# Kernel tuning notes

Hardware: AMD Instinct MI355X
Metric: run time of the kernel (lower is better)

Reference implementation:

```python
import jax, jax.numpy as jnp
import numpy as np
import math

L = 6      # num transformer layers
D = 128    # hidden_dim
H = 8      # heads
C = D // H # per-head dim (concat -> H*C == hidden_dim so residual add works)
F = 9      # node_features
OUT = 3    # output_dim
B, S, NN = 2, 128, 64
N = B * S * NN
E = 262144


def setup_inputs() -> dict:
    key = jax.random.key(0)
    ks = jax.random.split(key, 16)
    sc = 0.02
    g = lambda k, shp: jax.random.normal(k, shp, jnp.float32) * sc

    x = jax.random.normal(ks[0], (N, F), jnp.float32)
    edge_index = jax.random.randint(ks[1], (2, E), 0, N, dtype=jnp.int32)

    # sinusoidal positional encoding buffer [S, D]
    pos = np.arange(S, dtype=np.float32)[:, None]
    div = np.exp(np.arange(0, D, 2, dtype=np.float32) * (-math.log(10000.0) / D))
    pe = np.zeros((S, D), np.float32)
    pe[:, 0::2] = np.sin(pos * div)
    pe[:, 1::2] = np.cos(pos * div)

    return dict(
        x=x, edge_index=edge_index, pe=jnp.asarray(pe),
        Win=g(ks[2], (F, D)), bin_=jnp.zeros((D,), jnp.float32),
        Wq=g(ks[3], (L, D, D)), bq=jnp.zeros((L, D), jnp.float32),
        Wk=g(ks[4], (L, D, D)), bk=jnp.zeros((L, D), jnp.float32),
        Wv=g(ks[5], (L, D, D)), bv=jnp.zeros((L, D), jnp.float32),
        Ws=g(ks[6], (L, D, D)), bs=jnp.zeros((L, D), jnp.float32),
        Wb=g(ks[7], (L, 3 * D, 1)), bb=jnp.zeros((L, 1), jnp.float32),
        ln_g=jnp.ones((L, D), jnp.float32), ln_b=jnp.zeros((L, D), jnp.float32),
        Wo1=g(ks[8], (D, D // 2)), bo1=jnp.zeros((D // 2,), jnp.float32),
        Wo2=g(ks[9], (D // 2, OUT)), bo2=jnp.zeros((OUT,), jnp.float32),
        batch_size=B, seq_len=S, num_nodes=NN,
    )


def _layer_norm(x, g, b, eps=1e-5):
    mu = x.mean(-1, keepdims=True)
    var = ((x - mu) ** 2).mean(-1, keepdims=True)
    return (x - mu) / jnp.sqrt(var + eps) * g + b


def _transformer_conv(h, src, dst, Wq, bq, Wk, bk, Wv, bv, Ws, bs, Wb, bb):
    # PyG TransformerConv (beta=True, concat): edge gather -> per-head dot scores
    # -> scatter-softmax over incoming edges per dst node -> scatter-add aggregate.
    n = h.shape[0]
    q = (h @ Wq + bq).reshape(n, H, C)
    k = (h @ Wk + bk).reshape(n, H, C)
    v = (h @ Wv + bv).reshape(n, H, C)
    scores = jnp.einsum('ehc,ehc->eh', q[dst], k[src]) / math.sqrt(C)  # [E,H]
    m = jax.ops.segment_max(scores, dst, num_segments=n)               # [N,H]
    ex = jnp.exp(scores - jax.lax.stop_gradient(m)[dst])
    denom = jax.ops.segment_sum(ex, dst, num_segments=n)
    alpha = ex / (denom[dst] + 1e-16)                                  # [E,H]
    msg = (v[src] * alpha[:, :, None]).reshape(-1, H * C)              # [E,D]
    agg = jax.ops.segment_sum(msg, dst, num_segments=n)                # [N,D]
    xr = h @ Ws + bs                                                   # skip branch
    beta = jax.nn.sigmoid(jnp.concatenate([agg, xr, agg - xr], -1) @ Wb + bb)
    return beta * xr + (1.0 - beta) * agg


def reference(x, edge_index, pe, Win, bin_, Wq, bq, Wk, bk, Wv, bv, Ws, bs,
              Wb, bb, ln_g, ln_b, Wo1, bo1, Wo2, bo2,
              batch_size, seq_len, num_nodes):
    src, dst = edge_index[0], edge_index[1]
    d = Win.shape[1]
    h = x @ Win + bin_
    # add temporal positional encoding per timestep
    h = (h.reshape(batch_size, seq_len, num_nodes, d)
         + pe[:seq_len][None, :, None, :]).reshape(-1, d)
    for i in range(Wq.shape[0]):
        hn = _transformer_conv(h, src, dst, Wq[i], bq[i], Wk[i], bk[i],
                               Wv[i], bv[i], Ws[i], bs[i], Wb[i], bb[i])
        h = _layer_norm(h + hn, ln_g[i], ln_b[i])
    return jax.nn.relu(h @ Wo1 + bo1) @ Wo2 + bo2
```

## Files before the change

### kernel.cpp

```cpp
#include <hip/hip_runtime.h>

#define NNODES 16384
#define EDGES  262144
#define DH     128
#define NH     8
#define CH     16
#define NL     6
#define SEQ    128
#define NNPG   64

typedef short bf16x8 __attribute__((ext_vector_type(8)));
typedef float f32x4 __attribute__((ext_vector_type(4)));
typedef float f32x2 __attribute__((ext_vector_type(2)));

static __device__ __forceinline__ unsigned short f2bf(float f) {
  unsigned u = __float_as_uint(f);
  u += 0x7FFFu + ((u >> 16) & 1u);
  return (unsigned short)(u >> 16);
}
static __device__ __forceinline__ float bfl(unsigned u) { return __uint_as_float(u << 16); }
static __device__ __forceinline__ float bfh(unsigned u) { return __uint_as_float(u & 0xffff0000u); }
static __device__ __forceinline__ f32x2 mk2(float x, float y) { f32x2 t; t[0] = x; t[1] = y; return t; }

__global__ __launch_bounds__(128) void k_input(const float* __restrict__ x,
    const float* __restrict__ Win, const float* __restrict__ bin,
    const float* __restrict__ pe, float* __restrict__ h,
    unsigned short* __restrict__ hb) {
  const int n = blockIdx.x, d = threadIdx.x;
  __shared__ float xs[9];
  if (d < 9) xs[d] = x[n * 9 + d];
  __syncthreads();
  float acc = bin[d];
#pragma unroll
  for (int f = 0; f < 9; ++f) acc = fmaf(xs[f], Win[f * DH + d], acc);
  const float val = acc + pe[((n / NNPG) % SEQ) * DH + d];
  h[n * DH + d] = val;
  hb[n * DH + d] = f2bf(val);
}

__global__ __launch_bounds__(256) void k_count(const int* __restrict__ ei,
                                               int* __restrict__ cnt) {
  const int e = blockIdx.x * 256 + threadIdx.x;
  atomicAdd(&cnt[ei[EDGES + e]], 1);
}

__global__ __launch_bounds__(1024) void k_scan(int* __restrict__ cnt,
                                               int* __restrict__ row_start) {
  __shared__ int part[1024];
  const int t = threadIdx.x;
  int loc[16];
  int s = 0;
  const int base = t * 16;
#pragma unroll
  for (int i = 0; i < 16; ++i) { loc[i] = cnt[base + i]; s += loc[i]; }
  part[t] = s;
  __syncthreads();
  for (int off = 1; off < 1024; off <<= 1) {
    int add = (t >= off) ? part[t - off] : 0;
    __syncthreads();
    part[t] += add;
    __syncthreads();
  }
  int run = (t == 0) ? 0 : part[t - 1];
#pragma unroll
  for (int i = 0; i < 16; ++i) {
    row_start[base + i] = run;
    run += loc[i];
    cnt[base + i] = 0;
  }
  if (t == 0) row_start[NNODES] = EDGES;
}

__global__ __launch_bounds__(256) void k_fill(const int* __restrict__ ei,
    const int* __restrict__ row_start, int* __restrict__ cursor,
    int* __restrict__ csr_src) {
  const int e = blockIdx.x * 256 + threadIdx.x;
  const int d = ei[EDGES + e];
  csr_src[row_start[d] + atomicAdd(&cursor[d], 1)] = ei[e];
}

__global__ __launch_bounds__(64) void k_wconv(const float* __restrict__ Wq,
    const float* __restrict__ Wk, const float* __restrict__ Wv,
    const float* __restrict__ Ws, unsigned short* __restrict__ Wf) {
  const int bid = blockIdx.x;
  const int layer = bid >> 7, rem = bid & 127;
  const int mat = rem >> 5, tile = rem & 31;
  const int nt = tile >> 2, kt = tile & 3;
  const int lane = threadIdx.x;
  const float* W = ((mat == 0) ? Wq : (mat == 1) ? Wk : (mat == 2) ? Wv : Ws)
                   + layer * DH * DH;
  const int n = nt * 16 + (lane & 15);
  const int k0 = kt * 32 + (lane >> 4) * 8;
  unsigned pk[4];
#pragma unroll
  for (int jj = 0; jj < 4; ++jj) {
    const unsigned lo = f2bf(W[(k0 + 2 * jj) * DH + n]);
    const unsigned hi = f2bf(W[(k0 + 2 * jj + 1) * DH + n]);
    pk[jj] = lo | (hi << 16);
  }
  uint4 o = {pk[0], pk[1], pk[2], pk[3]};
  *(uint4*)&Wf[(((layer * 4 + mat) * 32 + tile) * 64 + lane) * 8] = o;
}

__global__ __launch_bounds__(256) void k_gemm(const unsigned short* __restrict__ hb,
    const unsigned short* __restrict__ Wf,
    const float* __restrict__ bq, const float* __restrict__ bk,
    const float* __restrict__ bv, const float* __restrict__ bs,
    unsigned short* __restrict__ qb, unsigned char* __restrict__ kv8,
    float* __restrict__ xr) {
  const int mt = blockIdx.x;
  const int wv = threadIdx.x >> 6, lane = threadIdx.x & 63;
  const int g = blockIdx.y * 4 + wv;
  const int mat = g >> 1, nbase = (g & 1) * 64;
  const unsigned short* Wm = Wf + mat * 16384;
  const float* bias = (mat == 0) ? bq : (mat == 1) ? bk : (mat == 2) ? bv : bs;
  const int m0 = lane & 15, quad = lane >> 4;
  const int nt0 = (g & 1) * 4;

  const f32x4 z = {0.f, 0.f, 0.f, 0.f};
  f32x4 acc[2][4] = {{z, z, z, z}, {z, z, z, z}};
#pragma unroll
  for (int kt = 0; kt < 4; ++kt) {
    const bf16x8 a0 = *(const bf16x8*)&hb[(mt * 32 + m0) * DH + kt * 32 + quad * 8];
    const bf16x8 a1 = *(const bf16x8*)&hb[(mt * 32 + 16 + m0) * DH + kt * 32 + quad * 8];
#pragma unroll
    for (int j = 0; j < 4; ++j) {
      const bf16x8 b = *(const bf16x8*)&Wm[(((nt0 + j) * 4 + kt) * 64 + lane) * 8];
      acc[0][j] = __builtin_amdgcn_mfma_f32_16x16x32_bf16(a0, b, acc[0][j], 0, 0, 0);
      acc[1][j] = __builtin_amdgcn_mfma_f32_16x16x32_bf16(a1, b, acc[1][j], 0, 0, 0);
    }
  }
  const int kvoff = (mat == 1) ? 0 : 128;
#pragma unroll
  for (int half = 0; half < 2; ++half) {
#pragma unroll
    for (int j = 0; j < 4; ++j) {
      const int col = nbase + j * 16 + m0;
      const float bvv = bias[col];
#pragma unroll
      for (int r = 0; r < 4; ++r) {
        const float val = acc[half][j][r] + bvv;
        const int row = mt * 32 + half * 16 + quad * 4 + r;
        if (mat == 0) {
          qb[row * DH + col] = f2bf(val);
        } else if (mat == 3) {
          xr[row * DH + col] = val;
        } else {
          const float nbv = __shfl_xor(val, 1);
          if ((lane & 1) == 0) {
            const int pk = __builtin_amdgcn_cvt_pk_fp8_f32(val, nbv, 0, false);
            *(unsigned short*)&kv8[row * 256 + kvoff + col] = (unsigned short)pk;
          }
        }
      }
    }
  }
}

__device__ __forceinline__ void load16bf2(const unsigned short* __restrict__ p, f32x2* r) {
  const uint4 a = *(const uint4*)p;
  const uint4 b = *(const uint4*)(p + 8);
  r[0] = mk2(bfl(a.x), bfh(a.x)); r[1] = mk2(bfl(a.y), bfh(a.y));
  r[2] = mk2(bfl(a.z), bfh(a.z)); r[3] = mk2(bfl(a.w), bfh(a.w));
  r[4] = mk2(bfl(b.x), bfh(b.x)); r[5] = mk2(bfl(b.y), bfh(b.y));
  r[6] = mk2(bfl(b.z), bfh(b.z)); r[7] = mk2(bfl(b.w), bfh(b.w));
}

__device__ __forceinline__ void decode8x2(const uint4 u, f32x2* r) {
  r[0] = __builtin_amdgcn_cvt_pk_f32_fp8(u.x, false);
  r[1] = __builtin_amdgcn_cvt_pk_f32_fp8(u.x, true);
  r[2] = __builtin_amdgcn_cvt_pk_f32_fp8(u.y, false);
  r[3] = __builtin_amdgcn_cvt_pk_f32_fp8(u.y, true);
  r[4] = __builtin_amdgcn_cvt_pk_f32_fp8(u.z, false);
  r[5] = __builtin_amdgcn_cvt_pk_f32_fp8(u.z, true);
  r[6] = __builtin_amdgcn_cvt_pk_f32_fp8(u.w, false);
  r[7] = __builtin_amdgcn_cvt_pk_f32_fp8(u.w, true);
}

__device__ __forceinline__ void edge_acc2(const uint4 ku, const uint4 vu, bool valid,
    const f32x2* __restrict__ q2, f32x2* __restrict__ a2, float& denom) {
  f32x2 kr[8];
  decode8x2(ku, kr);
  f32x2 d2 = mk2(0.f, 0.f);
#pragma unroll
  for (int c = 0; c < 8; ++c) d2 = d2 + q2[c] * kr[c];
  const float dot = d2[0] + d2[1];
  const float ex = valid ? __expf(dot * 0.25f) : 0.f;
  denom += ex;
  f32x2 vr[8];
  decode8x2(vu, vr);
  const f32x2 e2 = mk2(ex, ex);
#pragma unroll
  for (int c = 0; c < 8; ++c) a2[c] = a2[c] + e2 * vr[c];
}

__global__ __launch_bounds__(256, 4) void k_attn_epi(const unsigned short* __restrict__ qb,
    const unsigned char* __restrict__ kv8,
    const int* __restrict__ row_start, const int* __restrict__ csr_src,
    float* __restrict__ h, unsigned short* __restrict__ hb,
    const float* __restrict__ xr,
    const float* __restrict__ Wb, const float* __restrict__ bb,
    const float* __restrict__ ln_g, const float* __restrict__ ln_b) {
  const int wv = threadIdx.x >> 6, lane = threadIdx.x & 63;
  const int n = blockIdx.x * 4 + wv;
  const int es = lane >> 3, hd = lane & 7;
  const int beg = row_start[n], end = row_start[n + 1];
  const int deg = end - beg;
  const int ntb = (deg >= 32) ? 4 : ((deg + 7) >> 3);
  const int j0 = beg + es;
  int idx[4];
#pragma unroll
  for (int t = 0; t < 4; ++t) {
    idx[t] = -1;
    if (t < ntb) {
      const int jt = j0 + 8 * t;
      if (jt < end) idx[t] = csr_src[jt];
    }
  }
  f32x2 q2[8];
  load16bf2(&qb[n * DH + hd * CH], q2);
  uint4 kf[4], vf[4];
#pragma unroll
  for (int t = 0; t < 4; ++t) {
    if (t < ntb) {
      const int s = (idx[t] >= 0) ? idx[t] : 0;
      const unsigned char* base = &kv8[s * 256 + hd * CH];
      kf[t] = *(const uint4*)base;
      vf[t] = *(const uint4*)(base + 128);
    }
  }
  f32x2 a2[8];
#pragma unroll
  for (int c = 0; c < 8; ++c) a2[c] = mk2(0.f, 0.f);
  float denom = 0.f;
#pragma unroll
  for (int t = 0; t < 4; ++t) {
    if (t < ntb) edge_acc2(kf[t], vf[t], idx[t] >= 0, q2, a2, denom);
  }
  for (int j = j0 + 32; j < end; j += 8) {
    const int s = csr_src[j];
    const unsigned char* base = &kv8[s * 256 + hd * CH];
    const uint4 ku = *(const uint4*)base;
    const uint4 vu = *(const uint4*)(base + 128);
    edge_acc2(ku, vu, true, q2, a2, denom);
  }
#pragma unroll
  for (int off = 8; off <= 32; off <<= 1) {
    denom += __shfl_xor(denom, off);
#pragma unroll
    for (int c = 0; c < 8; ++c) {
      const f32x2 t = mk2(__shfl_xor(a2[c][0], off), __shfl_xor(a2[c][1], off));
      a2[c] = a2[c] + t;
    }
  }
  const float inv = 1.f / (denom + 1e-16f);
  float o0 = 0.f, o1 = 0.f;
#pragma unroll
  for (int c = 0; c < 8; ++c) {
    if (es == c) { o0 = a2[c][0]; o1 = a2[c][1]; }
  }
  const int d0 = hd * CH + es * 2;
  const float ax = o0 * inv, ay = o1 * inv;
  const float2 r = *(const float2*)&xr[n * DH + d0];
  const float2 w0 = *(const float2*)&Wb[d0];
  const float2 w1 = *(const float2*)&Wb[DH + d0];
  const float2 w2 = *(const float2*)&Wb[2 * DH + d0];
  float p = ax * w0.x + ay * w0.y + r.x * w1.x + r.y * w1.y
          + (ax - r.x) * w2.x + (ay - r.y) * w2.y;
#pragma unroll
  for (int off = 1; off <= 32; off <<= 1) p += __shfl_xor(p, off);
  const float beta = 1.f / (1.f + __expf(-(p + bb[0])));
  const float2 hv = *(const float2*)&h[n * DH + d0];
  const float t0 = hv.x + beta * r.x + (1.f - beta) * ax;
  const float t1 = hv.y + beta * r.y + (1.f - beta) * ay;
  float sum = t0 + t1, sq = t0 * t0 + t1 * t1;
#pragma unroll
  for (int off = 1; off <= 32; off <<= 1) {
    sum += __shfl_xor(sum, off);
    sq  += __shfl_xor(sq, off);
  }
  const float mu = sum * (1.f / DH);
  const float rinv = rsqrtf(sq * (1.f / DH) - mu * mu + 1e-5f);
  const float2 g = *(const float2*)&ln_g[d0];
  const float2 b = *(const float2*)&ln_b[d0];
  float2 o = {(t0 - mu) * rinv * g.x + b.x, (t1 - mu) * rinv * g.y + b.y};
  *(float2*)&h[n * DH + d0] = o;
  const unsigned lo = f2bf(o.x), hi = f2bf(o.y);
  *(unsigned*)&hb[n * DH + d0] = lo | (hi << 16);
}

__global__ __launch_bounds__(256) void k_final(const float* __restrict__ h,
    const float* __restrict__ Wo1, const float* __restrict__ bo1,
    const float* __restrict__ Wo2, const float* __restrict__ bo2,
    float* __restrict__ out) {
  __shared__ float hs[4][DH];
  const int lane = threadIdx.x & 63, wid = threadIdx.x >> 6;
  const int n = blockIdx.x * 4 + wid;
  const float2 hv = *(const float2*)&h[n * DH + lane * 2];
  hs[wid][lane * 2] = hv.x;
  hs[wid][lane * 2 + 1] = hv.y;
  __syncthreads();
  float m = bo1[lane];
#pragma unroll 16
  for (int d = 0; d < DH; ++d) m = fmaf(hs[wid][d], Wo1[d * 64 + lane], m);
  m = fmaxf(m, 0.f);
  float o0 = m * Wo2[lane * 3 + 0];
  float o1 = m * Wo2[lane * 3 + 1];
  float o2 = m * Wo2[lane * 3 + 2];
#pragma unroll
  for (int off = 32; off; off >>= 1) {
    o0 += __shfl_xor(o0, off);
    o1 += __shfl_xor(o1, off);
    o2 += __shfl_xor(o2, off);
  }
  if (lane == 0) {
    out[n * 3 + 0] = o0 + bo2[0];
    out[n * 3 + 1] = o1 + bo2[1];
    out[n * 3 + 2] = o2 + bo2[2];
  }
}

extern "C" void kernel_launch(void* const* d_in, const int* in_sizes, int n_in,
                              void* d_out, int out_size, void* d_ws, size_t ws_size,
                              hipStream_t stream) {
  const float* x   = (const float*)d_in[0];
  const int*   ei  = (const int*)d_in[1];
  const float* pe  = (const float*)d_in[2];
  const float* Win = (const float*)d_in[3];
  const float* bin = (const float*)d_in[4];
  const float* Wq  = (const float*)d_in[5];
  const float* bq  = (const float*)d_in[6];
  const float* Wk  = (const float*)d_in[7];
  const float* bk  = (const float*)d_in[8];
  const float* Wv  = (const float*)d_in[9];
  const float* bv  = (const float*)d_in[10];
  const float* Wsk = (const float*)d_in[11];
  const float* bs  = (const float*)d_in[12];
  const float* Wb  = (const float*)d_in[13];
  const float* bb  = (const float*)d_in[14];
  const float* lng = (const float*)d_in[15];
  const float* lnb = (const float*)d_in[16];
  const float* Wo1 = (const float*)d_in[17];
  const float* bo1 = (const float*)d_in[18];
  const float* Wo2 = (const float*)d_in[19];
  const float* bo2 = (const float*)d_in[20];

  const size_t NU = (size_t)NNODES * DH;
  char* base = (char*)d_ws;
  float* h   = (float*)base;                  base += NU * 4;
  float* xr  = (float*)base;                  base += NU * 4;
  unsigned short* hb = (unsigned short*)base; base += NU * 2;
  unsigned short* qb = (unsigned short*)base; base += NU * 2;
  unsigned char* kv8 = (unsigned char*)base;  base += NU * 2;
  unsigned short* Wf = (unsigned short*)base; base += (size_t)NL * 4 * 16384 * 2;
  int* row_start = (int*)base;                base += (NNODES + 1) * 4;
  int* cnt       = (int*)base;                base += NNODES * 4;
  int* csr_src   = (int*)base;

  (void)hipMemsetAsync(cnt, 0, NNODES * sizeof(int), stream);
  k_count<<<EDGES / 256, 256, 0, stream>>>(ei, cnt);
  k_scan<<<1, 1024, 0, stream>>>(cnt, row_start);
  k_fill<<<EDGES / 256, 256, 0, stream>>>(ei, row_start, cnt, csr_src);
  k_wconv<<<NL * 128, 64, 0, stream>>>(Wq, Wk, Wv, Wsk, Wf);
  k_input<<<NNODES, 128, 0, stream>>>(x, Win, bin, pe, h, hb);
  for (int l = 0; l < NL; ++l) {
    k_gemm<<<dim3(NNODES / 32, 2), 256, 0, stream>>>(
        hb, Wf + (size_t)l * 4 * 16384,
        bq + l * DH, bk + l * DH, bv + l * DH, bs + l * DH, qb, kv8, xr);
    k_attn_epi<<<NNODES / 4, 256, 0, stream>>>(qb, kv8, row_start, csr_src,
                                               h, hb, xr, Wb + l * 3 * DH, bb + l,
                                               lng + l * DH, lnb + l * DH);
  }
  k_final<<<NNODES / 4, 256, 0, stream>>>(h, Wo1, bo1, Wo2, bo2, (float*)d_out);
}
```

Baseline: 379.5 us.

## Interleave K/V per head, pad first-32 CSR neighbors, warp-shuffle scan and reduce-scatter

Replaces the shared-memory Hillis-Steele scan with a warp-shuffle scan plus per-wave sums. It adds a padded per-node table of the first 32 neighbor indices, so each attention lane fetches its four indices with one int4 load. It also interleaves the fp8 K and V per head so both sit in the same 32-byte chunk, and swaps the butterfly all-reduce of the 16 accumulator values for a halving reduce-scatter that moves fewer shuffles. The cost is an extra memset and padded index buffer, plus a nondeterministic slot order within the padded table.

Result: no change. 376.4 us (-0.8%).

```diff
diff --git a/kernel.cpp b/kernel.cpp
--- a/kernel.cpp
+++ b/kernel.cpp
@@ -46,22 +46,29 @@
 
 __global__ __launch_bounds__(1024) void k_scan(int* __restrict__ cnt,
                                                int* __restrict__ row_start) {
-  __shared__ int part[1024];
+  __shared__ int wsum[16];
   const int t = threadIdx.x;
+  const int lane = t & 63, wid = t >> 6;
   int loc[16];
   int s = 0;
   const int base = t * 16;
 #pragma unroll
   for (int i = 0; i < 16; ++i) { loc[i] = cnt[base + i]; s += loc[i]; }
-  part[t] = s;
+  int sc = s;
+#pragma unroll
+  for (int off = 1; off <= 32; off <<= 1) {
+    const int v = __shfl_up(sc, off);
+    if (lane >= off) sc += v;
+  }
+  if (lane == 63) wsum[wid] = sc;
   __syncthreads();
-  for (int off = 1; off < 1024; off <<= 1) {
-    int add = (t >= off) ? part[t - off] : 0;
-    __syncthreads();
-    part[t] += add;
-    __syncthreads();
-  }
-  int run = (t == 0) ? 0 : part[t - 1];
+  int wbase = 0;
+#pragma unroll
+  for (int w = 0; w < 16; ++w) {
+    const int v = wsum[w];
+    if (w < wid) wbase += v;
+  }
+  int run = wbase + sc - s;
 #pragma unroll
   for (int i = 0; i < 16; ++i) {
     row_start[base + i] = run;
@@ -73,10 +80,13 @@
 
 __global__ __launch_bounds__(256) void k_fill(const int* __restrict__ ei,
     const int* __restrict__ row_start, int* __restrict__ cursor,
-    int* __restrict__ csr_src) {
+    int* __restrict__ csr_src, int* __restrict__ csr_pad) {
   const int e = blockIdx.x * 256 + threadIdx.x;
   const int d = ei[EDGES + e];
-  csr_src[row_start[d] + atomicAdd(&cursor[d], 1)] = ei[e];
+  const int s = ei[e];
+  const int slot = atomicAdd(&cursor[d], 1);
+  csr_src[row_start[d] + slot] = s;
+  if (slot < 32) csr_pad[d * 32 + (slot & 7) * 4 + (slot >> 3)] = s;
 }
 
 __global__ __launch_bounds__(64) void k_wconv(const float* __restrict__ Wq,
@@ -130,7 +140,7 @@
       acc[1][j] = __builtin_amdgcn_mfma_f32_16x16x32_bf16(a1, b, acc[1][j], 0, 0, 0);
     }
   }
-  const int kvoff = (mat == 1) ? 0 : 128;
+  const int kvoff = (mat == 1) ? 0 : 16;
 #pragma unroll
   for (int half = 0; half < 2; ++half) {
 #pragma unroll
@@ -149,7 +159,9 @@
           const float nbv = __shfl_xor(val, 1);
           if ((lane & 1) == 0) {
             const int pk = __builtin_amdgcn_cvt_pk_fp8_f32(val, nbv, 0, false);
-            *(unsigned short*)&kv8[row * 256 + kvoff + col] = (unsigned short)pk;
+            const int head = col >> 4, dim = col & 15;
+            *(unsigned short*)&kv8[row * 256 + head * 32 + kvoff + dim] =
+                (unsigned short)pk;
           }
         }
       }
@@ -197,6 +209,7 @@
 __global__ __launch_bounds__(256, 4) void k_attn_epi(const unsigned short* __restrict__ qb,
     const unsigned char* __restrict__ kv8,
     const int* __restrict__ row_start, const int* __restrict__ csr_src,
+    const int* __restrict__ csr_pad,
     float* __restrict__ h, unsigned short* __restrict__ hb,
     const float* __restrict__ xr,
     const float* __restrict__ Wb, const float* __restrict__ bb,
@@ -204,19 +217,11 @@
   const int wv = threadIdx.x >> 6, lane = threadIdx.x & 63;
   const int n = blockIdx.x * 4 + wv;
   const int es = lane >> 3, hd = lane & 7;
+  const int4 iv = *(const int4*)&csr_pad[n * 32 + es * 4];
   const int beg = row_start[n], end = row_start[n + 1];
   const int deg = end - beg;
   const int ntb = (deg >= 32) ? 4 : ((deg + 7) >> 3);
-  const int j0 = beg + es;
-  int idx[4];
-#pragma unroll
-  for (int t = 0; t < 4; ++t) {
-    idx[t] = -1;
-    if (t < ntb) {
-      const int jt = j0 + 8 * t;
-      if (jt < end) idx[t] = csr_src[jt];
-    }
-  }
+  int idx[4] = {iv.x, iv.y, iv.z, iv.w};
   f32x2 q2[8];
   load16bf2(&qb[n * DH + hd * CH], q2);
   uint4 kf[4], vf[4];
@@ -224,9 +229,9 @@
   for (int t = 0; t < 4; ++t) {
     if (t < ntb) {
       const int s = (idx[t] >= 0) ? idx[t] : 0;
-      const unsigned char* base = &kv8[s * 256 + hd * CH];
+      const unsigned char* base = &kv8[s * 256 + hd * 32];
       kf[t] = *(const uint4*)base;
-      vf[t] = *(const uint4*)(base + 128);
+      vf[t] = *(const uint4*)(base + 16);
     }
   }
   f32x2 a2[8];
@@ -237,28 +242,42 @@
   for (int t = 0; t < 4; ++t) {
     if (t < ntb) edge_acc2(kf[t], vf[t], idx[t] >= 0, q2, a2, denom);
   }
-  for (int j = j0 + 32; j < end; j += 8) {
+  for (int j = beg + es + 32; j < end; j += 8) {
     const int s = csr_src[j];
-    const unsigned char* base = &kv8[s * 256 + hd * CH];
+    const unsigned char* base = &kv8[s * 256 + hd * 32];
     const uint4 ku = *(const uint4*)base;
-    const uint4 vu = *(const uint4*)(base + 128);
+    const uint4 vu = *(const uint4*)(base + 16);
     edge_acc2(ku, vu, true, q2, a2, denom);
   }
 #pragma unroll
-  for (int off = 8; off <= 32; off <<= 1) {
-    denom += __shfl_xor(denom, off);
-#pragma unroll
-    for (int c = 0; c < 8; ++c) {
-      const f32x2 t = mk2(__shfl_xor(a2[c][0], off), __shfl_xor(a2[c][1], off));
-      a2[c] = a2[c] + t;
-    }
-  }
+  for (int off = 8; off <= 32; off <<= 1) denom += __shfl_xor(denom, off);
+  const bool hi32 = (lane & 32) != 0;
+  f32x2 r4[4];
+#pragma unroll
+  for (int c = 0; c < 4; ++c) {
+    const f32x2 keep = hi32 ? a2[c + 4] : a2[c];
+    const f32x2 send = hi32 ? a2[c] : a2[c + 4];
+    const f32x2 rec = mk2(__shfl_xor(send[0], 32), __shfl_xor(send[1], 32));
+    r4[c] = keep + rec;
+  }
+  const bool hi16 = (lane & 16) != 0;
+  f32x2 r2[2];
+#pragma unroll
+  for (int c = 0; c < 2; ++c) {
+    const f32x2 keep = hi16 ? r4[c + 2] : r4[c];
+    const f32x2 send = hi16 ? r4[c] : r4[c + 2];
+    const f32x2 rec = mk2(__shfl_xor(send[0], 16), __shfl_xor(send[1], 16));
+    r2[c] = keep + rec;
+  }
+  const bool hi8 = (lane & 8) != 0;
+  {
+    const f32x2 keep = hi8 ? r2[1] : r2[0];
+    const f32x2 send = hi8 ? r2[0] : r2[1];
+    const f32x2 rec = mk2(__shfl_xor(send[0], 8), __shfl_xor(send[1], 8));
+    r2[0] = keep + rec;
+  }
+  const float o0 = r2[0][0], o1 = r2[0][1];
   const float inv = 1.f / (denom + 1e-16f);
-  float o0 = 0.f, o1 = 0.f;
-#pragma unroll
-  for (int c = 0; c < 8; ++c) {
-    if (es == c) { o0 = a2[c][0]; o1 = a2[c][1]; }
-  }
   const int d0 = hd * CH + es * 2;
   const float ax = o0 * inv, ay = o1 * inv;
   const float2 r = *(const float2*)&xr[n * DH + d0];
@@ -355,19 +374,21 @@
   unsigned short* Wf = (unsigned short*)base; base += (size_t)NL * 4 * 16384 * 2;
   int* row_start = (int*)base;                base += (NNODES + 1) * 4;
   int* cnt       = (int*)base;                base += NNODES * 4;
-  int* csr_src   = (int*)base;
+  int* csr_src   = (int*)base;                base += (size_t)EDGES * 4;
+  int* csr_pad   = (int*)base;                base += (size_t)NNODES * 32 * 4;
 
   (void)hipMemsetAsync(cnt, 0, NNODES * sizeof(int), stream);
+  (void)hipMemsetAsync(csr_pad, 0xFF, (size_t)NNODES * 32 * sizeof(int), stream);
   k_count<<<EDGES / 256, 256, 0, stream>>>(ei, cnt);
   k_scan<<<1, 1024, 0, stream>>>(cnt, row_start);
-  k_fill<<<EDGES / 256, 256, 0, stream>>>(ei, row_start, cnt, csr_src);
+  k_fill<<<EDGES / 256, 256, 0, stream>>>(ei, row_start, cnt, csr_src, csr_pad);
   k_wconv<<<NL * 128, 64, 0, stream>>>(Wq, Wk, Wv, Wsk, Wf);
   k_input<<<NNODES, 128, 0, stream>>>(x, Win, bin, pe, h, hb);
   for (int l = 0; l < NL; ++l) {
     k_gemm<<<dim3(NNODES / 32, 2), 256, 0, stream>>>(
         hb, Wf + (size_t)l * 4 * 16384,
         bq + l * DH, bk + l * DH, bv + l * DH, bs + l * DH, qb, kv8, xr);
-    k_attn_epi<<<NNODES / 4, 256, 0, stream>>>(qb, kv8, row_start, csr_src,
+    k_attn_epi<<<NNODES / 4, 256, 0, stream>>>(qb, kv8, row_start, csr_src, csr_pad,
                                                h, hb, xr, Wb + l * 3 * DH, bb + l,
                                                lng + l * DH, lnb + l * DH);
   }
```
